# Kernel optimization log

Measured on AMD Instinct MI355X. Metric: run time of the kernel, lower is better.

The kernel has to match this reference:

```python
import jax, jax.numpy as jnp
import numpy as np


def setup_inputs() -> dict:
    key = jax.random.key(0)
    ks = jax.random.split(key, 6)
    B, C, H, W = 2, 256, 128, 512
    img1 = jax.random.normal(ks[0], (B, C, H, W), jnp.float32)
    img2 = jax.random.normal(ks[1], (B, C, H, W), jnp.float32)
    intri1 = jax.random.uniform(ks[2], (B, 3, 3), jnp.float32)
    intri2 = jax.random.uniform(ks[3], (B, 3, 3), jnp.float32)
    extri1 = jax.random.uniform(ks[4], (B, 4, 4), jnp.float32)
    extri2 = jax.random.uniform(ks[5], (B, 4, 4), jnp.float32)
    return {"img1": img1, "img2": img2, "intri1": intri1, "intri2": intri2,
            "extri1": extri1, "extri2": extri2}


TEMPERATURE = 1.0  # init default
DISP_CLAMP = 0.1   # from corresp_prob_to_depth_conf


def reference(img1, img2, intri1, intri2, extri1, extri2):
    """CostVolume(dot, dual=False, pack_lr=False, geometry_mask=True).forward.
    Returns (depth, confidence), each (B, 1, H, W). G=1 group dim kept.
    """
    B, C, H, W = img1.shape
    # full per-row correlation volume: vol[b,h,w1,w2] = <img1[:,w1], img2[:,w2]> / sqrt(C)
    vol = jnp.einsum('bchw,bchv->bhwv', img1, img2) / jnp.asarray(np.sqrt(C), img1.dtype)
    idx = jnp.arange(W, dtype=vol.dtype)
    # left_first=True -> lower-triangular geometry mask (correspondence w2 <= w1)
    tril = (idx[None, :] <= idx[:, None]).astype(vol.dtype)  # (W1, W2)
    # NOTE: mask is applied AFTER softmax (prob is NOT renormalized), as in source
    prob = jax.nn.softmax(vol / TEMPERATURE, axis=-1) * tril  # (B,H,W1,W2)
    corresp = jnp.sum(prob * idx, axis=-1)[:, None]  # soft-argmax index, (B,1,H,W)
    confidence = jnp.max(prob, axis=-1)[:, None]      # (B,1,H,W)
    # corresp2disp with normalize=True (normalized_intri default True)
    disp = jnp.abs(corresp - idx) / W
    disp = jnp.clip(disp, DISP_CLAMP)
    # d2d_transform (reconstructed): pinhole disparity->depth, depth = fx * baseline / disp
    fx = intri1[:, 0, 0][:, None, None, None]
    baseline = jnp.linalg.norm(extri1[:, :3, 3] - extri2[:, :3, 3], axis=-1)[:, None, None, None]
    depth = fx * baseline / disp
    return depth, confidence
```

## Files before the change

### kernel.cpp

```cpp
#include <hip/hip_runtime.h>
#include <hip/hip_bf16.h>

typedef __attribute__((ext_vector_type(4))) float f32x4;
typedef __attribute__((ext_vector_type(8))) short s16x8;

#define C_DIM 256
#define H_DIM 128
#define W_DIM 512
#define HW    (H_DIM * W_DIM)
#define CHW   (C_DIM * HW)
#define WS_NEED (2ull * 128 * 512 * 256 * 2)

__device__ __forceinline__ unsigned short f2bf(float f) {
    return __builtin_bit_cast(unsigned short, __float2bfloat16(f));
}

__device__ __forceinline__ void gl_lds16(const void* g, void* l) {
    __builtin_amdgcn_global_load_lds(
        (const __attribute__((address_space(1))) void*)g,
        (__attribute__((address_space(3))) void*)l, 16, 0, 0);
}

__global__ __launch_bounds__(256) void transpose_kernel(
    const float* __restrict__ img2, unsigned short* __restrict__ bws)
{
    __shared__ unsigned short tile[64][65];
    const int t = threadIdx.x;
    const int d = blockIdx.x;
    const int cb = d & 3, wb = (d >> 2) & 7, bh = d >> 5;
    const int b = bh >> 7, h = bh & 127;
    const float* src = img2 + (size_t)b * CHW + (size_t)h * W_DIM
                            + (size_t)(cb * 64) * HW + wb * 64;
    {
        const int c = t >> 2, w0 = (t & 3) << 4;
        const float* p = src + (size_t)c * HW + w0;
        #pragma unroll
        for (int i = 0; i < 16; i += 4) {
            f32x4 v = *(const f32x4*)(p + i);
            #pragma unroll
            for (int j = 0; j < 4; ++j) tile[c][w0 + i + j] = f2bf(v[j]);
        }
    }
    __syncthreads();
    {
        const int n_l = t >> 2, c4 = (t & 3) << 4;
        unsigned short vals[16];
        #pragma unroll
        for (int i = 0; i < 16; ++i) vals[i] = tile[c4 + i][n_l];
        unsigned short* dst = bws + ((size_t)bh * 512 + wb * 64 + n_l) * 256 + cb * 64 + c4;
        *(s16x8*)(dst)     = *(s16x8*)&vals[0];
        *(s16x8*)(dst + 8) = *(s16x8*)&vals[8];
    }
}

__global__ __launch_bounds__(512, 2) void costvol_kernel(
    const float* __restrict__ img1, const unsigned short* __restrict__ bws,
    const float* __restrict__ intri1,
    const float* __restrict__ extri1, const float* __restrict__ extri2,
    float* __restrict__ out)
{
    __shared__ __align__(16) unsigned char smem[98304];
    unsigned short* Alds = (unsigned short*)smem;

    const int t = threadIdx.x;
    const int d = blockIdx.x;
    const int win = d >> 6, pos = d & 63;
    const int bh    = win * 8 + (pos & 7);
    const int w1blk = pos >> 3;
    const int b = bh >> 7, h = bh & 127;
    const int w1base = w1blk * 64;

    const int wv = t >> 6, lane = t & 63;
    const int lrow = lane & 15, hq = lane >> 4;

    const int n_st  = (lane >> 2);
    const int k8_st = lane & 3;
    const unsigned short* bsrc[4];
    #pragma unroll
    for (int i = 0; i < 4; ++i) {
        const int n = (wv * 4 + i) * 16 + n_st;
        bsrc[i] = bws + ((size_t)bh * 512 + n) * 256 + 8 * (k8_st ^ ((n >> 1) & 3));
    }

    #pragma unroll
    for (int i = 0; i < 4; ++i)
        gl_lds16(bsrc[i], smem + 32768 + (wv * 4 + i) * 1024);

    const float* i1 = img1 + (size_t)b * CHW + (size_t)h * W_DIM;
    {
        const int c    = t >> 1;
        const int wseg = (t & 1) << 5;
        const float* src = i1 + (size_t)c * HW + (size_t)(w1base + wseg);
        #pragma unroll
        for (int i0 = 0; i0 < 32; i0 += 4) {
            f32x4 v = *(const f32x4*)(src + i0);
            #pragma unroll
            for (int j = 0; j < 4; ++j) {
                const int w = wseg + i0 + j;
                Alds[w * 256 + ((((c >> 3) ^ (w & 15)) << 3) | (c & 7))] = f2bf(v[j] * 0.0625f);
            }
        }
    }
    __syncthreads();

    const int wn = wv;
    f32x4 acc[4][4] = {};

    int boff[4];
    #pragma unroll
    for (int w2t = 0; w2t < 4; ++w2t) {
        const int n = 64 * wn + 16 * w2t + lrow;
        boff[w2t] = n * 64 + 16 * (hq ^ ((n >> 1) & 3));
    }

    #pragma unroll
    for (int kc = 0; kc < 8; ++kc) {
        if (kc < 7) {
            const int nb = (kc + 1) & 1;
            #pragma unroll
            for (int i = 0; i < 4; ++i)
                gl_lds16(bsrc[i] + (kc + 1) * 32, smem + 32768 + nb * 32768 + (wv * 4 + i) * 1024);
        }
        const unsigned char* Bbuf = smem + 32768 + (kc & 1) * 32768;
        s16x8 afr[4];
        #pragma unroll
        for (int w1t = 0; w1t < 4; ++w1t) {
            const int row = 16 * w1t + lrow;
            const int kb  = (kc << 2) + hq;
            afr[w1t] = *(const s16x8*)&Alds[row * 256 + ((kb ^ (row & 15)) << 3)];
        }
        #pragma unroll
        for (int w2t = 0; w2t < 4; ++w2t) {
            const s16x8 bfr = *(const s16x8*)(Bbuf + boff[w2t]);
            #pragma unroll
            for (int w1t = 0; w1t < 4; ++w1t)
                acc[w2t][w1t] = __builtin_amdgcn_mfma_f32_16x16x32_bf16(
                    bfr, afr[w1t], acc[w2t][w1t], 0, 0, 0);
        }
        __syncthreads();
    }

    float (*red)[64][3] = (float(*)[64][3])smem;
    #pragma unroll
    for (int w1t = 0; w1t < 4; ++w1t) {
        const int w1l = 16 * w1t + lrow;
        const int w1g = w1base + w1l;
        float Se = 0.f, Sei = 0.f, Me = 0.f;
        #pragma unroll
        for (int w2t = 0; w2t < 4; ++w2t) {
            #pragma unroll
            for (int r = 0; r < 4; ++r) {
                const int w2 = 64 * wn + 16 * w2t + 4 * hq + r;
                const float e = __expf(acc[w2t][w1t][r]);
                Se += e;
                if (w2 <= w1g) { Sei += e * (float)w2; Me = fmaxf(Me, e); }
            }
        }
        Se  += __shfl_xor(Se, 16, 64);  Se  += __shfl_xor(Se, 32, 64);
        Sei += __shfl_xor(Sei, 16, 64); Sei += __shfl_xor(Sei, 32, 64);
        Me = fmaxf(Me, __shfl_xor(Me, 16, 64)); Me = fmaxf(Me, __shfl_xor(Me, 32, 64));
        if (hq == 0) {
            red[wn][w1l][0] = Se;
            red[wn][w1l][1] = Sei;
            red[wn][w1l][2] = Me;
        }
    }
    __syncthreads();

    if (t < 64) {
        const int row = t;
        float Se = 0.f, Sei = 0.f, Me = 0.f;
        #pragma unroll
        for (int q = 0; q < 8; ++q) {
            Se  += red[q][row][0];
            Sei += red[q][row][1];
            Me   = fmaxf(Me, red[q][row][2]);
        }
        const int w1g = w1base + row;
        const float corresp = Sei / Se;
        const float conf    = Me / Se;
        float disp = fabsf(corresp - (float)w1g) * (1.0f / 512.0f);
        disp = fmaxf(disp, 0.1f);
        const float fx = intri1[b * 9];
        const float dx = extri1[b * 16 + 3]  - extri2[b * 16 + 3];
        const float dy = extri1[b * 16 + 7]  - extri2[b * 16 + 7];
        const float dz = extri1[b * 16 + 11] - extri2[b * 16 + 11];
        const float bl = sqrtf(dx * dx + dy * dy + dz * dz);
        const float depth = fx * bl / disp;
        const int oidx = b * HW + h * W_DIM + w1g;
        out[oidx]          = depth;
        out[2 * HW + oidx] = conf;
    }
}

__global__ __launch_bounds__(512, 4) void costvol_fallback(
    const float* __restrict__ img1, const float* __restrict__ img2,
    const float* __restrict__ intri1,
    const float* __restrict__ extri1, const float* __restrict__ extri2,
    float* __restrict__ out)
{
    __shared__ __align__(16) unsigned char smem[32768];
    unsigned short* Alds = (unsigned short*)smem;
    const int t = threadIdx.x;
    const int d = blockIdx.x;
    const int win = d >> 6, pos = d & 63;
    const int bh    = win * 8 + (pos & 7);
    const int w1blk = pos >> 3;
    const int b = bh >> 7, h = bh & 127;
    const int w1base = w1blk * 64;
    const float* i1 = img1 + (size_t)b * CHW + (size_t)h * W_DIM;
    const float* i2 = img2 + (size_t)b * CHW + (size_t)h * W_DIM;
    {
        const int c    = t >> 1;
        const int wseg = (t & 1) << 5;
        const float* src = i1 + (size_t)c * HW + (size_t)(w1base + wseg);
        #pragma unroll
        for (int i0 = 0; i0 < 32; i0 += 4) {
            f32x4 v = *(const f32x4*)(src + i0);
            #pragma unroll
            for (int j = 0; j < 4; ++j) {
                const int w = wseg + i0 + j;
                Alds[w * 256 + ((((c >> 3) ^ (w & 15)) << 3) | (c & 7))] = f2bf(v[j]);
            }
        }
    }
    __syncthreads();
    const int wn = t >> 6, lane = t & 63;
    const int lrow = lane & 15, hq = lane >> 4;
    const float* pb[4];
    #pragma unroll
    for (int ct = 0; ct < 4; ++ct)
        pb[ct] = i2 + (size_t)(8 * hq) * HW + (64 * wn + 16 * ct + lrow);
    f32x4 acc[4][4] = {};
    for (int kc = 0; kc < 8; ++kc) {
        s16x8 afr[4];
        #pragma unroll
        for (int rt = 0; rt < 4; ++rt) {
            const int row = 16 * rt + lrow;
            const int kb  = (kc << 2) + hq;
            afr[rt] = *(const s16x8*)&Alds[row * 256 + ((kb ^ (row & 15)) << 3)];
        }
        #pragma unroll
        for (int ct = 0; ct < 4; ++ct) {
            const float* p = pb[ct] + (size_t)(32 * kc) * HW;
            float f[8];
            #pragma unroll
            for (int j = 0; j < 8; ++j) f[j] = p[(size_t)j * HW];
            s16x8 bfr;
            #pragma unroll
            for (int j = 0; j < 8; ++j) bfr[j] = (short)f2bf(f[j]);
            #pragma unroll
            for (int rt = 0; rt < 4; ++rt)
                acc[rt][ct] = __builtin_amdgcn_mfma_f32_16x16x32_bf16(afr[rt], bfr, acc[rt][ct], 0, 0, 0);
        }
    }
    __syncthreads();
    float (*red)[64][3] = (float(*)[64][3])smem;
    #pragma unroll
    for (int rt = 0; rt < 4; ++rt) {
        #pragma unroll
        for (int r = 0; r < 4; ++r) {
            const int row = 16 * rt + 4 * hq + r;
            const int w1g = w1base + row;
            float Se = 0.f, Sei = 0.f, Me = 0.f;
            #pragma unroll
            for (int ct = 0; ct < 4; ++ct) {
                const int col = 64 * wn + 16 * ct + lrow;
                const float e = __expf(acc[rt][ct][r] * 0.0625f);
                Se += e;
                if (col <= w1g) { Sei += e * (float)col; Me = fmaxf(Me, e); }
            }
            #pragma unroll
            for (int m = 1; m < 16; m <<= 1) {
                Se  += __shfl_xor(Se,  m, 64);
                Sei += __shfl_xor(Sei, m, 64);
                Me   = fmaxf(Me, __shfl_xor(Me, m, 64));
            }
            if (lrow == 0) { red[wn][row][0] = Se; red[wn][row][1] = Sei; red[wn][row][2] = Me; }
        }
    }
    __syncthreads();
    if (t < 64) {
        const int row = t;
        float Se = 0.f, Sei = 0.f, Me = 0.f;
        #pragma unroll
        for (int q = 0; q < 8; ++q) {
            Se += red[q][row][0]; Sei += red[q][row][1]; Me = fmaxf(Me, red[q][row][2]);
        }
        const int w1g = w1base + row;
        const float corresp = Sei / Se;
        const float conf    = Me / Se;
        float disp = fabsf(corresp - (float)w1g) * (1.0f / 512.0f);
        disp = fmaxf(disp, 0.1f);
        const float fx = intri1[b * 9];
        const float dx = extri1[b * 16 + 3]  - extri2[b * 16 + 3];
        const float dy = extri1[b * 16 + 7]  - extri2[b * 16 + 7];
        const float dz = extri1[b * 16 + 11] - extri2[b * 16 + 11];
        const float bl = sqrtf(dx * dx + dy * dy + dz * dz);
        const int oidx = b * HW + h * W_DIM + w1g;
        out[oidx]          = fx * bl / disp;
        out[2 * HW + oidx] = conf;
    }
}

extern "C" void kernel_launch(void* const* d_in, const int* in_sizes, int n_in,
                              void* d_out, int out_size, void* d_ws, size_t ws_size,
                              hipStream_t stream) {
    const float* img1   = (const float*)d_in[0];
    const float* img2   = (const float*)d_in[1];
    const float* intri1 = (const float*)d_in[2];
    const float* extri1 = (const float*)d_in[4];
    const float* extri2 = (const float*)d_in[5];
    if (ws_size >= WS_NEED) {
        unsigned short* bws = (unsigned short*)d_ws;
        transpose_kernel<<<dim3(8192), dim3(256), 0, stream>>>(img2, bws);
        costvol_kernel<<<dim3(2048), dim3(512), 0, stream>>>(
            img1, bws, intri1, extri1, extri2, (float*)d_out);
    } else {
        costvol_fallback<<<dim3(2048), dim3(512), 0, stream>>>(
            img1, img2, intri1, extri1, extri2, (float*)d_out);
    }
}
```

Measured before the change: 141.8 us.

## Double the w1 tile per block to 128 rows with 1024-thread blocks

```diff
diff --git a/kernel.cpp b/kernel.cpp
--- a/kernel.cpp
+++ b/kernel.cpp
@@ -53,63 +53,61 @@
     }
 }
 
-__global__ __launch_bounds__(512, 2) void costvol_kernel(
+__global__ __launch_bounds__(1024, 4) void costvol_kernel(
     const float* __restrict__ img1, const unsigned short* __restrict__ bws,
     const float* __restrict__ intri1,
     const float* __restrict__ extri1, const float* __restrict__ extri2,
     float* __restrict__ out)
 {
-    __shared__ __align__(16) unsigned char smem[98304];
+    __shared__ __align__(16) unsigned char smem[131072];
     unsigned short* Alds = (unsigned short*)smem;
 
     const int t = threadIdx.x;
     const int d = blockIdx.x;
-    const int win = d >> 6, pos = d & 63;
-    const int bh    = win * 8 + (pos & 7);
+    const int pos = d & 31;
+    const int bh    = (d >> 5) * 8 + (pos & 7);
     const int w1blk = pos >> 3;
     const int b = bh >> 7, h = bh & 127;
-    const int w1base = w1blk * 64;
+    const int w1base = w1blk * 128;
 
     const int wv = t >> 6, lane = t & 63;
     const int lrow = lane & 15, hq = lane >> 4;
 
-    const int n_st  = (lane >> 2);
-    const int k8_st = lane & 3;
-    const unsigned short* bsrc[4];
-    #pragma unroll
-    for (int i = 0; i < 4; ++i) {
-        const int n = (wv * 4 + i) * 16 + n_st;
-        bsrc[i] = bws + ((size_t)bh * 512 + n) * 256 + 8 * (k8_st ^ ((n >> 1) & 3));
-    }
-
-    #pragma unroll
-    for (int i = 0; i < 4; ++i)
-        gl_lds16(bsrc[i], smem + 32768 + (wv * 4 + i) * 1024);
+    const unsigned short* bsrc[2];
+    #pragma unroll
+    for (int i = 0; i < 2; ++i) {
+        const int u  = t + i * 1024;
+        const int n  = u >> 2, k8 = u & 3;
+        bsrc[i] = bws + ((size_t)bh * 512 + n) * 256 + 8 * (k8 ^ ((n >> 1) & 3));
+    }
+
+    #pragma unroll
+    for (int i = 0; i < 2; ++i)
+        gl_lds16(bsrc[i], smem + 65536 + i * 16384 + wv * 1024);
 
     const float* i1 = img1 + (size_t)b * CHW + (size_t)h * W_DIM;
     {
-        const int c    = t >> 1;
-        const int wseg = (t & 1) << 5;
-        const float* src = i1 + (size_t)c * HW + (size_t)(w1base + wseg);
+        const int c  = t >> 2;
+        const int w0 = (t & 3) << 5;
+        const float* src = i1 + (size_t)c * HW + (size_t)(w1base + w0);
         #pragma unroll
         for (int i0 = 0; i0 < 32; i0 += 4) {
             f32x4 v = *(const f32x4*)(src + i0);
             #pragma unroll
             for (int j = 0; j < 4; ++j) {
-                const int w = wseg + i0 + j;
+                const int w = w0 + i0 + j;
                 Alds[w * 256 + ((((c >> 3) ^ (w & 15)) << 3) | (c & 7))] = f2bf(v[j] * 0.0625f);
             }
         }
     }
     __syncthreads();
 
-    const int wn = wv;
-    f32x4 acc[4][4] = {};
-
-    int boff[4];
-    #pragma unroll
-    for (int w2t = 0; w2t < 4; ++w2t) {
-        const int n = 64 * wn + 16 * w2t + lrow;
+    f32x4 acc[2][8] = {};
+
+    int boff[2];
+    #pragma unroll
+    for (int w2t = 0; w2t < 2; ++w2t) {
+        const int n = 32 * wv + 16 * w2t + lrow;
         boff[w2t] = n * 64 + 16 * (hq ^ ((n >> 1) & 3));
     }
 
@@ -118,39 +116,38 @@
         if (kc < 7) {
             const int nb = (kc + 1) & 1;
             #pragma unroll
-            for (int i = 0; i < 4; ++i)
-                gl_lds16(bsrc[i] + (kc + 1) * 32, smem + 32768 + nb * 32768 + (wv * 4 + i) * 1024);
-        }
-        const unsigned char* Bbuf = smem + 32768 + (kc & 1) * 32768;
-        s16x8 afr[4];
-        #pragma unroll
-        for (int w1t = 0; w1t < 4; ++w1t) {
+            for (int i = 0; i < 2; ++i)
+                gl_lds16(bsrc[i] + (kc + 1) * 32, smem + 65536 + nb * 32768 + i * 16384 + wv * 1024);
+        }
+        const unsigned char* Bbuf = smem + 65536 + (kc & 1) * 32768;
+        s16x8 bfr[2];
+        #pragma unroll
+        for (int w2t = 0; w2t < 2; ++w2t)
+            bfr[w2t] = *(const s16x8*)(Bbuf + boff[w2t]);
+        #pragma unroll
+        for (int w1t = 0; w1t < 8; ++w1t) {
             const int row = 16 * w1t + lrow;
             const int kb  = (kc << 2) + hq;
-            afr[w1t] = *(const s16x8*)&Alds[row * 256 + ((kb ^ (row & 15)) << 3)];
-        }
-        #pragma unroll
-        for (int w2t = 0; w2t < 4; ++w2t) {
-            const s16x8 bfr = *(const s16x8*)(Bbuf + boff[w2t]);
-            #pragma unroll
-            for (int w1t = 0; w1t < 4; ++w1t)
+            const s16x8 afr = *(const s16x8*)&Alds[row * 256 + ((kb ^ (row & 15)) << 3)];
+            #pragma unroll
+            for (int w2t = 0; w2t < 2; ++w2t)
                 acc[w2t][w1t] = __builtin_amdgcn_mfma_f32_16x16x32_bf16(
-                    bfr, afr[w1t], acc[w2t][w1t], 0, 0, 0);
+                    bfr[w2t], afr, acc[w2t][w1t], 0, 0, 0);
         }
         __syncthreads();
     }
 
-    float (*red)[64][3] = (float(*)[64][3])smem;
-    #pragma unroll
-    for (int w1t = 0; w1t < 4; ++w1t) {
+    float (*red)[128][3] = (float(*)[128][3])smem;
+    #pragma unroll
+    for (int w1t = 0; w1t < 8; ++w1t) {
         const int w1l = 16 * w1t + lrow;
         const int w1g = w1base + w1l;
         float Se = 0.f, Sei = 0.f, Me = 0.f;
         #pragma unroll
-        for (int w2t = 0; w2t < 4; ++w2t) {
+        for (int w2t = 0; w2t < 2; ++w2t) {
             #pragma unroll
             for (int r = 0; r < 4; ++r) {
-                const int w2 = 64 * wn + 16 * w2t + 4 * hq + r;
+                const int w2 = 32 * wv + 16 * w2t + 4 * hq + r;
                 const float e = __expf(acc[w2t][w1t][r]);
                 Se += e;
                 if (w2 <= w1g) { Sei += e * (float)w2; Me = fmaxf(Me, e); }
@@ -160,18 +157,18 @@
         Sei += __shfl_xor(Sei, 16, 64); Sei += __shfl_xor(Sei, 32, 64);
         Me = fmaxf(Me, __shfl_xor(Me, 16, 64)); Me = fmaxf(Me, __shfl_xor(Me, 32, 64));
         if (hq == 0) {
-            red[wn][w1l][0] = Se;
-            red[wn][w1l][1] = Sei;
-            red[wn][w1l][2] = Me;
-        }
-    }
-    __syncthreads();
-
-    if (t < 64) {
+            red[wv][w1l][0] = Se;
+            red[wv][w1l][1] = Sei;
+            red[wv][w1l][2] = Me;
+        }
+    }
+    __syncthreads();
+
+    if (t < 128) {
         const int row = t;
         float Se = 0.f, Sei = 0.f, Me = 0.f;
         #pragma unroll
-        for (int q = 0; q < 8; ++q) {
+        for (int q = 0; q < 16; ++q) {
             Se  += red[q][row][0];
             Sei += red[q][row][1];
             Me   = fmaxf(Me, red[q][row][2]);
@@ -314,7 +311,7 @@
     if (ws_size >= WS_NEED) {
         unsigned short* bws = (unsigned short*)d_ws;
         transpose_kernel<<<dim3(8192), dim3(256), 0, stream>>>(img2, bws);
-        costvol_kernel<<<dim3(2048), dim3(512), 0, stream>>>(
+        costvol_kernel<<<dim3(1024), dim3(1024), 0, stream>>>(
             img1, bws, intri1, extri1, extri2, (float*)d_out);
     } else {
         costvol_fallback<<<dim3(2048), dim3(512), 0, stream>>>(
```

Result: faster. 123.7 us (-12.8%).

## Single-buffer B in per-wave LDS slices, drop per-chunk block barriers

Applied to the files above, without the earlier changes.

```diff
diff --git a/kernel.cpp b/kernel.cpp
--- a/kernel.cpp
+++ b/kernel.cpp
@@ -53,13 +53,13 @@
     }
 }
 
-__global__ __launch_bounds__(512, 2) void costvol_kernel(
+__global__ __launch_bounds__(512, 4) void costvol_kernel(
     const float* __restrict__ img1, const unsigned short* __restrict__ bws,
     const float* __restrict__ intri1,
     const float* __restrict__ extri1, const float* __restrict__ extri2,
     float* __restrict__ out)
 {
-    __shared__ __align__(16) unsigned char smem[98304];
+    __shared__ __align__(16) unsigned char smem[65536];
     unsigned short* Alds = (unsigned short*)smem;
 
     const int t = threadIdx.x;
@@ -73,18 +73,14 @@
     const int wv = t >> 6, lane = t & 63;
     const int lrow = lane & 15, hq = lane >> 4;
 
-    const int n_st  = (lane >> 2);
-    const int k8_st = lane & 3;
-    const unsigned short* bsrc[4];
-    #pragma unroll
-    for (int i = 0; i < 4; ++i) {
-        const int n = (wv * 4 + i) * 16 + n_st;
-        bsrc[i] = bws + ((size_t)bh * 512 + n) * 256 + 8 * (k8_st ^ ((n >> 1) & 3));
-    }
+    const unsigned short* bsrc0 =
+        bws + ((size_t)bh * 512 + 64 * wv + (lane >> 2)) * 256
+            + 8 * ((lane & 3) ^ ((lane >> 3) & 3));
+    unsigned char* const bdst = smem + 32768 + wv * 4096;
 
     #pragma unroll
     for (int i = 0; i < 4; ++i)
-        gl_lds16(bsrc[i], smem + 32768 + (wv * 4 + i) * 1024);
+        gl_lds16(bsrc0 + i * 4096, bdst + i * 1024);
 
     const float* i1 = img1 + (size_t)b * CHW + (size_t)h * W_DIM;
     {
@@ -103,42 +99,44 @@
     }
     __syncthreads();
 
-    const int wn = wv;
     f32x4 acc[4][4] = {};
 
     int boff[4];
     #pragma unroll
-    for (int w2t = 0; w2t < 4; ++w2t) {
-        const int n = 64 * wn + 16 * w2t + lrow;
-        boff[w2t] = n * 64 + 16 * (hq ^ ((n >> 1) & 3));
-    }
+    for (int w2t = 0; w2t < 4; ++w2t)
+        boff[w2t] = (16 * w2t + lrow) * 64 + 16 * (hq ^ ((lrow >> 1) & 3));
 
     #pragma unroll
     for (int kc = 0; kc < 8; ++kc) {
-        if (kc < 7) {
-            const int nb = (kc + 1) & 1;
-            #pragma unroll
-            for (int i = 0; i < 4; ++i)
-                gl_lds16(bsrc[i] + (kc + 1) * 32, smem + 32768 + nb * 32768 + (wv * 4 + i) * 1024);
-        }
-        const unsigned char* Bbuf = smem + 32768 + (kc & 1) * 32768;
-        s16x8 afr[4];
+        s16x8 bfr[4], afr[4];
+        #pragma unroll
+        for (int w2t = 0; w2t < 4; ++w2t)
+            bfr[w2t] = *(const s16x8*)(bdst + boff[w2t]);
         #pragma unroll
         for (int w1t = 0; w1t < 4; ++w1t) {
             const int row = 16 * w1t + lrow;
             const int kb  = (kc << 2) + hq;
             afr[w1t] = *(const s16x8*)&Alds[row * 256 + ((kb ^ (row & 15)) << 3)];
         }
-        #pragma unroll
-        for (int w2t = 0; w2t < 4; ++w2t) {
-            const s16x8 bfr = *(const s16x8*)(Bbuf + boff[w2t]);
+        asm volatile("s_waitcnt lgkmcnt(0)" ::: "memory");
+        __builtin_amdgcn_sched_barrier(0);
+        if (kc < 7) {
+            #pragma unroll
+            for (int i = 0; i < 4; ++i)
+                gl_lds16(bsrc0 + (kc + 1) * 32 + i * 4096, bdst + i * 1024);
+        }
+        __builtin_amdgcn_sched_barrier(0);
+        #pragma unroll
+        for (int w2t = 0; w2t < 4; ++w2t)
             #pragma unroll
             for (int w1t = 0; w1t < 4; ++w1t)
                 acc[w2t][w1t] = __builtin_amdgcn_mfma_f32_16x16x32_bf16(
-                    bfr, afr[w1t], acc[w2t][w1t], 0, 0, 0);
-        }
-        __syncthreads();
-    }
+                    bfr[w2t], afr[w1t], acc[w2t][w1t], 0, 0, 0);
+        if (kc < 7)
+            asm volatile("s_waitcnt vmcnt(0)" ::: "memory");
+    }
+
+    __syncthreads();
 
     float (*red)[64][3] = (float(*)[64][3])smem;
     #pragma unroll
@@ -150,7 +148,7 @@
         for (int w2t = 0; w2t < 4; ++w2t) {
             #pragma unroll
             for (int r = 0; r < 4; ++r) {
-                const int w2 = 64 * wn + 16 * w2t + 4 * hq + r;
+                const int w2 = 64 * wv + 16 * w2t + 4 * hq + r;
                 const float e = __expf(acc[w2t][w1t][r]);
                 Se += e;
                 if (w2 <= w1g) { Sei += e * (float)w2; Me = fmaxf(Me, e); }
@@ -160,9 +158,9 @@
         Sei += __shfl_xor(Sei, 16, 64); Sei += __shfl_xor(Sei, 32, 64);
         Me = fmaxf(Me, __shfl_xor(Me, 16, 64)); Me = fmaxf(Me, __shfl_xor(Me, 32, 64));
         if (hq == 0) {
-            red[wn][w1l][0] = Se;
-            red[wn][w1l][1] = Sei;
-            red[wn][w1l][2] = Me;
+            red[wv][w1l][0] = Se;
+            red[wv][w1l][1] = Sei;
+            red[wv][w1l][2] = Me;
         }
     }
     __syncthreads();
```

Result: faster. 122.8 us, median of 2 (-13.4%).
